# Kernel optimization log

Measured on AMD Instinct MI355X. Metric: run time of the kernel, lower is better.

Reference implementation:

```python
import jax, jax.numpy as jnp
import numpy as np

B, NQ, S, D = 8, 1024, 2048, 512

def setup_inputs() -> dict:
    key = jax.random.key(0)
    k1, k2, k3, k4 = jax.random.split(key, 4)
    queries = jax.random.normal(k1, (B, NQ, D), dtype=jnp.float32)
    keys = jax.random.normal(k2, (B, S, D), dtype=jnp.float32)
    values = jax.random.normal(k3, (B, S, D), dtype=jnp.float32)
    mask = jax.random.randint(k4, (B, NQ, S), 0, 2, dtype=jnp.int32)
    return {"queries": queries, "keys": keys, "values": values, "mask": mask}

def reference(queries, keys, values, mask):
    # scores: dot-product attention scores (b, nq, s)
    scores = jnp.einsum('bqd,bsd->bqs', queries, keys)
    attention_dist = jax.nn.softmax(scores, axis=2)
    # mask then renormalize over seq axis
    attention_dist = attention_dist * mask.astype(attention_dist.dtype)
    attention_dist = attention_dist / attention_dist.sum(axis=2, keepdims=True)
    # weighted sum of values: equivalent to (dist.unsqueeze(3) * values.unsqueeze(1)).sum(2)
    final_vector = jnp.einsum('bqs,bsd->bqd', attention_dist, values)
    return final_vector
```

## Files before the change

### kernel.cpp

```cpp
#include <hip/hip_runtime.h>


#define Bz 8
#define NQz 1024
#define Sz 2048
#define Dz 512
#define QTT 128
#define TS 32
#define KP 520
#define PP 40

typedef _Float16 f16x8 __attribute__((ext_vector_type(8)));
typedef float f32x4 __attribute__((ext_vector_type(4)));
typedef unsigned short ushort_t;

#define AS1(p) ((const __attribute__((address_space(1))) unsigned int*)(p))
#define AS3(p) ((__attribute__((address_space(3))) unsigned int*)(p))
#define DRAIN_ALL() __builtin_amdgcn_s_waitcnt(0)

__device__ __forceinline__ ushort_t f2h(float x) {
  _Float16 h = (_Float16)x;
  return __builtin_bit_cast(ushort_t, h);
}
__device__ __forceinline__ float h2f(ushort_t u) {
  return (float)__builtin_bit_cast(_Float16, u);
}

__global__ __launch_bounds__(256)
void prep(const float* __restrict__ K, const float* __restrict__ V,
          const int* __restrict__ Mi, ushort_t* __restrict__ Kf,
          ushort_t* __restrict__ Vt, unsigned* __restrict__ Mp) {
  __shared__ ushort_t sT[64][41];
  const int t = threadIdx.x;
  int bx = blockIdx.x;
  if (bx < 8192) {
    size_t e = ((size_t)bx * 256 + t) * 4;
    float4 v = *(const float4*)(K + e);
    uint2 w;
    w.x = (unsigned)f2h(v.x) | ((unsigned)f2h(v.y) << 16);
    w.y = (unsigned)f2h(v.z) | ((unsigned)f2h(v.w) << 16);
    *(uint2*)(Kf + e) = w;
    return;
  }
  bx -= 8192;
  if (bx < 4096) {
    const int b = bx >> 9;
    const int rest = bx & 511;
    const int st = rest >> 4;
    const int dt = rest & 15;
    const int s0 = st * 64, d0 = dt * 32;
    const float* Vb = V + ((size_t)b * Sz + s0) * Dz + d0;
#pragma unroll
    for (int i = 0; i < 2; ++i) {
      int idx = t + 256 * i;
      int s = idx >> 3;
      int dc = (idx & 7) * 4;
      float4 v = *(const float4*)(Vb + (size_t)s * Dz + dc);
      uint2 w;
      w.x = (unsigned)f2h(v.x) | ((unsigned)f2h(v.y) << 16);
      w.y = (unsigned)f2h(v.z) | ((unsigned)f2h(v.w) << 16);
      *(uint2*)(&sT[s][dc]) = w;
    }
    __syncthreads();
    ushort_t* VtB = Vt + ((size_t)b * Dz + d0) * Sz + s0;
    int d = t >> 3, c = t & 7;
    uint4 u;
    ushort_t* tp = (ushort_t*)&u;
#pragma unroll
    for (int j = 0; j < 8; ++j) tp[j] = sT[c * 8 + j][d];
    *(uint4*)(VtB + (size_t)d * Sz + c * 8) = u;
    return;
  }
  bx -= 4096;
  const int lane = t & 63;
  const size_t base = (size_t)bx * 1024 + t * 4;
  const int4 mv = *(const int4*)(Mi + base);
  unsigned nib = (mv.x ? 1u : 0u) | (mv.y ? 2u : 0u) |
                 (mv.z ? 4u : 0u) | (mv.w ? 8u : 0u);
  unsigned v = nib << ((lane & 7) * 4);
  v |= __shfl_xor(v, 1);
  v |= __shfl_xor(v, 2);
  v |= __shfl_xor(v, 4);
  if ((lane & 7) == 0) Mp[bx * 32 + (t >> 3)] = v;
}

template <int SPLIT>
__global__ __launch_bounds__(512, 2)
void attn_flash(const float* __restrict__ Q, const unsigned* __restrict__ Mp,
                const ushort_t* __restrict__ Kf, const ushort_t* __restrict__ Vt,
                ushort_t* __restrict__ Opart, float* __restrict__ Mpart,
                float* __restrict__ Lpart) {
  __shared__ ushort_t sK[2][TS][KP];
  __shared__ ushort_t sV[2][Dz][TS];
  __shared__ ushort_t sP[8][16][PP];

  const int tid  = threadIdx.x;
  const int wave = tid >> 6;
  const int lane = tid & 63;
  const int l16  = lane & 15;
  const int quad = lane >> 4;

  const int bxr = blockIdx.x;
  const int b   = bxr & 7;
  const int rest = bxr >> 3;
  const int qt  = rest / SPLIT;
  const int sh  = rest % SPLIT;
  const int q0  = qt * QTT;
  const int SLEN = Sz / SPLIT;
  const int NTt  = SLEN / TS;
  const int sbeg = sh * SLEN;
  const int qw   = q0 + wave * 16;

  const float*    Qb  = Q  + ((size_t)b * NQz + qw) * Dz;
  const ushort_t* KfB = Kf + (size_t)b * Sz * Dz;
  const ushort_t* VtB = Vt + (size_t)b * Dz * Sz;
  const unsigned* MpB = Mp + ((size_t)b * NQz + qw) * (Sz / 32);

  const int vql  = (lane & 3) ^ ((lane >> 3) & 3);
  const int vcol = (quad ^ ((l16 >> 1) & 3)) * 8;

  auto issue_tile = [&](int s0n, int bsel) {
#pragma unroll
    for (int j = 0; j < 4; ++j) {
      int row = wave * 4 + j;
      const ushort_t* gp = KfB + (size_t)(s0n + row) * Dz + lane * 8;
      __builtin_amdgcn_global_load_lds(AS1(gp), AS3(&sK[bsel][row][0]), 16, 0, 0);
    }
#pragma unroll
    for (int j = 0; j < 4; ++j) {
      int dbase = wave * 64 + j * 16;
      int d = dbase + (lane >> 2);
      const ushort_t* gp = VtB + (size_t)d * Sz + s0n + vql * 8;
      __builtin_amdgcn_global_load_lds(AS1(gp), AS3(&sV[bsel][dbase][0]), 16, 0, 0);
    }
  };
  auto load_mask = [&](int s0n) -> unsigned {
    return MpB[(size_t)l16 * (Sz / 32) + (s0n >> 5)];
  };

  issue_tile(sbeg, 0);
  unsigned msk_cur = load_mask(sbeg);

  f16x8 qa[16];
  {
    const float* qrow = Qb + (size_t)l16 * Dz;
#pragma unroll
    for (int kk = 0; kk < 16; ++kk) {
      const float4 a = *(const float4*)(qrow + kk * 32 + quad * 8);
      const float4 c = *(const float4*)(qrow + kk * 32 + quad * 8 + 4);
      f16x8 h;
      h[0] = (_Float16)a.x; h[1] = (_Float16)a.y;
      h[2] = (_Float16)a.z; h[3] = (_Float16)a.w;
      h[4] = (_Float16)c.x; h[5] = (_Float16)c.y;
      h[6] = (_Float16)c.z; h[7] = (_Float16)c.w;
      qa[kk] = h;
    }
  }
  if (NTt > 1) issue_tile(sbeg + TS, 1);
  DRAIN_ALL();
  __syncthreads();

  float m_ln = -1e30f, l_ln = 0.0f;
  f32x4 oacc[32];
#pragma unroll
  for (int nt = 0; nt < 32; ++nt) oacc[nt] = (f32x4){0.f, 0.f, 0.f, 0.f};

  const ushort_t* vbase0 = &sV[0][0][0] + (size_t)l16 * TS + vcol;
  const ushort_t* vbase1 = &sV[1][0][0] + (size_t)l16 * TS + vcol;

  for (int i = 0; i < NTt; ++i) {
    const int buf = i & 1;
    if (i) {
      DRAIN_ALL();
      __syncthreads();
      if (i + 1 < NTt) issue_tile(sbeg + (i + 1) * TS, buf ^ 1);
    }
    unsigned msk_nxt = (i + 1 < NTt) ? load_mask(sbeg + (i + 1) * TS) : 0u;

    f32x4 a00 = (f32x4){0.f,0.f,0.f,0.f}, a01 = (f32x4){0.f,0.f,0.f,0.f};
    f32x4 a10 = (f32x4){0.f,0.f,0.f,0.f}, a11 = (f32x4){0.f,0.f,0.f,0.f};
    {
      const ushort_t* kh0 = &sK[buf][l16][quad * 8];
      const ushort_t* kh1 = &sK[buf][16 + l16][quad * 8];
#pragma unroll
      for (int kk = 0; kk < 16; kk += 2) {
        f16x8 k00 = *(const f16x8*)(kh0 + kk * 32);
        f16x8 k10 = *(const f16x8*)(kh1 + kk * 32);
        f16x8 k01 = *(const f16x8*)(kh0 + kk * 32 + 32);
        f16x8 k11 = *(const f16x8*)(kh1 + kk * 32 + 32);
        a00 = __builtin_amdgcn_mfma_f32_16x16x32_f16(k00, qa[kk], a00, 0, 0, 0);
        a10 = __builtin_amdgcn_mfma_f32_16x16x32_f16(k10, qa[kk], a10, 0, 0, 0);
        a01 = __builtin_amdgcn_mfma_f32_16x16x32_f16(k01, qa[kk+1], a01, 0, 0, 0);
        a11 = __builtin_amdgcn_mfma_f32_16x16x32_f16(k11, qa[kk+1], a11, 0, 0, 0);
      }
    }
    f32x4 s0v, s1v;
#pragma unroll
    for (int r = 0; r < 4; ++r) { s0v[r] = a00[r] + a01[r]; s1v[r] = a10[r] + a11[r]; }

    const unsigned mb = msk_cur;
    float se0[4], se1[4];
#pragma unroll
    for (int r = 0; r < 4; ++r) {
      se0[r] = ((mb >> (quad * 4 + r)) & 1u)      ? s0v[r] : -1e30f;
      se1[r] = ((mb >> (16 + quad * 4 + r)) & 1u) ? s1v[r] : -1e30f;
    }
    float rmax = fmaxf(fmaxf(fmaxf(se0[0], se0[1]), fmaxf(se0[2], se0[3])),
                       fmaxf(fmaxf(se1[0], se1[1]), fmaxf(se1[2], se1[3])));
    rmax = fmaxf(rmax, __shfl_xor(rmax, 16));
    rmax = fmaxf(rmax, __shfl_xor(rmax, 32));

    ushort_t pb0[4], pb1[4];
    float rsum = 0.f;
#pragma unroll
    for (int r = 0; r < 4; ++r) {
      float p0 = ((mb >> (quad * 4 + r)) & 1u)      ? __expf(se0[r] - rmax) : 0.f;
      float p1 = ((mb >> (16 + quad * 4 + r)) & 1u) ? __expf(se1[r] - rmax) : 0.f;
      pb0[r] = f2h(p0); pb1[r] = f2h(p1);
      rsum += h2f(pb0[r]) + h2f(pb1[r]);
    }
    {
      uint2 w0, w1;
      w0.x = (unsigned)pb0[0] | ((unsigned)pb0[1] << 16);
      w0.y = (unsigned)pb0[2] | ((unsigned)pb0[3] << 16);
      w1.x = (unsigned)pb1[0] | ((unsigned)pb1[1] << 16);
      w1.y = (unsigned)pb1[2] | ((unsigned)pb1[3] << 16);
      *(uint2*)(&sP[wave][l16][quad * 4]) = w0;
      *(uint2*)(&sP[wave][l16][16 + quad * 4]) = w1;
    }
    rsum += __shfl_xor(rsum, 16);
    rsum += __shfl_xor(rsum, 32);

    float m_new = fmaxf(m_ln, rmax);
    float scl   = __expf(rmax - m_new);
    float al_ln = __expf(m_ln - m_new);
    bool  grw   = m_new > m_ln;
    l_ln = al_ln * l_ln + scl * rsum;
    m_ln = m_new;

    f16x8 praw = *(const f16x8*)(&sP[wave][l16][quad * 8]);
    f16x8 pa;
    {
      _Float16 sh16 = (_Float16)scl;
#pragma unroll
      for (int j = 0; j < 8; ++j) pa[j] = praw[j] * sh16;
    }

    if (__any((int)grw)) {
      float al[4];
#pragma unroll
      for (int r = 0; r < 4; ++r) al[r] = __shfl(al_ln, quad * 4 + r);
#pragma unroll
      for (int nt = 0; nt < 32; ++nt)
#pragma unroll
        for (int r = 0; r < 4; ++r) oacc[nt][r] *= al[r];
    }

    const ushort_t* vb_ = buf ? vbase1 : vbase0;
#pragma unroll
    for (int nt = 0; nt < 32; ++nt) {
      f16x8 vb = *(const f16x8*)(vb_ + nt * 512);
      oacc[nt] = __builtin_amdgcn_mfma_f32_16x16x32_f16(pa, vb, oacc[nt], 0, 0, 0);
    }

    msk_cur = msk_nxt;
  }

  const size_t rbase = (size_t)(b * SPLIT + sh) * NQz + q0 + wave * 16;
#pragma unroll
  for (int nt = 0; nt < 32; ++nt) {
#pragma unroll
    for (int r = 0; r < 4; ++r) {
      Opart[(rbase + quad * 4 + r) * Dz + nt * 16 + l16] = f2h(oacc[nt][r]);
    }
  }
  if (quad == 0) {
    Mpart[rbase + l16] = m_ln;
    Lpart[rbase + l16] = l_ln;
  }
}

template <int SPLIT>
__global__ __launch_bounds__(256)
void combine(const ushort_t* __restrict__ Opart, const float* __restrict__ Mpart,
             const float* __restrict__ Lpart, float* __restrict__ Out) {
  int gid = blockIdx.x * 256 + threadIdx.x;
  int row = gid >> 7;
  int b   = row >> 10;
  int q   = row & 1023;
  int c   = (gid & 127) * 4;
  float mv[SPLIT], lv[SPLIT];
  float m = -1e30f;
#pragma unroll
  for (int p = 0; p < SPLIT; ++p) {
    size_t ip = (size_t)(b * SPLIT + p) * NQz + q;
    mv[p] = Mpart[ip];
    lv[p] = Lpart[ip];
    m = fmaxf(m, mv[p]);
  }
  float w[SPLIT], denom = 0.f;
#pragma unroll
  for (int p = 0; p < SPLIT; ++p) {
    w[p] = __expf(mv[p] - m);
    denom += w[p] * lv[p];
  }
  float inv = 1.0f / denom;
  float4 o = {0.f, 0.f, 0.f, 0.f};
#pragma unroll
  for (int p = 0; p < SPLIT; ++p) {
    size_t ip = (size_t)(b * SPLIT + p) * NQz + q;
    const ushort_t* op = Opart + ip * Dz + c;
    uint2 raw = *(const uint2*)op;
    o.x += w[p] * h2f((ushort_t)(raw.x & 0xffff));
    o.y += w[p] * h2f((ushort_t)(raw.x >> 16));
    o.z += w[p] * h2f((ushort_t)(raw.y & 0xffff));
    o.w += w[p] * h2f((ushort_t)(raw.y >> 16));
  }
  o.x *= inv; o.y *= inv; o.z *= inv; o.w *= inv;
  *(float4*)(Out + ((size_t)b * NQz + q) * Dz + c) = o;
}

extern "C" void kernel_launch(void* const* d_in, const int* in_sizes, int n_in,
                              void* d_out, int out_size, void* d_ws, size_t ws_size,
                              hipStream_t stream) {
  const float* Q = (const float*)d_in[0];
  const float* K = (const float*)d_in[1];
  const float* V = (const float*)d_in[2];
  const int*   M = (const int*)d_in[3];
  float* O = (float*)d_out;

  const size_t NKV   = (size_t)Bz * Sz * Dz;
  const size_t maskW = (size_t)Bz * NQz * (Sz / 32);

  ushort_t* Kf = (ushort_t*)d_ws;
  ushort_t* Vt = Kf + NKV;
  unsigned* Mp = (unsigned*)(Vt + NKV);
  ushort_t* Opart = (ushort_t*)(Mp + maskW);

  auto need_bytes = [&](int S) -> size_t {
    return NKV * 2 * 2 + maskW * 4
         + (size_t)Bz * S * NQz * Dz * 2
         + (size_t)Bz * S * NQz * 4 * 2;
  };

  prep<<<dim3(28672), dim3(256), 0, stream>>>(K, V, M, Kf, Vt, Mp);

  if (ws_size >= need_bytes(4)) {
    constexpr int S = 4;
    float* Mpart = (float*)(Opart + (size_t)Bz * S * NQz * Dz);
    float* Lpart = Mpart + (size_t)Bz * S * NQz;
    attn_flash<S><<<dim3(8 * (NQz / QTT) * S), dim3(512), 0, stream>>>(
        Q, Mp, Kf, Vt, Opart, Mpart, Lpart);
    combine<S><<<dim3(4096), dim3(256), 0, stream>>>(Opart, Mpart, Lpart, O);
  } else {
    constexpr int S = 2;
    float* Mpart = (float*)(Opart + (size_t)Bz * S * NQz * Dz);
    float* Lpart = Mpart + (size_t)Bz * S * NQz;
    attn_flash<S><<<dim3(8 * (NQz / QTT) * S), dim3(512), 0, stream>>>(
        Q, Mp, Kf, Vt, Opart, Mpart, Lpart);
    combine<S><<<dim3(4096), dim3(256), 0, stream>>>(Opart, Mpart, Lpart, O);
  }
}
```

Before: 246.7 us.

## Shrink flash tiles to 16 keys, keep P in registers with 16x16x16 MFMA

Halves the query tile (4 waves of 16 rows) and the key tile (16 keys), so the PV product can take P directly from the QK accumulator layout via the 16x16x16 f16 MFMA. This removes the per-wave shared-memory round trip for P. The mask word is now loaded every other tile, softmax scaling uses the running max directly, and MFMA sections are wrapped in s_setprio. The trade-off is smaller tiles: twice as many barrier iterations, and K/V tiles are reused by fewer query rows per block, which raises LDS and global traffic per FLOP. The smaller MFMA shape also does less work per instruction.

```diff
diff --git a/kernel.cpp b/kernel.cpp
--- a/kernel.cpp
+++ b/kernel.cpp
@@ -5,12 +5,12 @@
 #define NQz 1024
 #define Sz 2048
 #define Dz 512
-#define QTT 128
-#define TS 32
+#define QTT 64
+#define TS 16
 #define KP 520
-#define PP 40
 
 typedef _Float16 f16x8 __attribute__((ext_vector_type(8)));
+typedef _Float16 f16x4 __attribute__((ext_vector_type(4)));
 typedef float f32x4 __attribute__((ext_vector_type(4)));
 typedef unsigned short ushort_t;
 
@@ -85,14 +85,13 @@
 }
 
 template <int SPLIT>
-__global__ __launch_bounds__(512, 2)
+__global__ __launch_bounds__(256, 2)
 void attn_flash(const float* __restrict__ Q, const unsigned* __restrict__ Mp,
                 const ushort_t* __restrict__ Kf, const ushort_t* __restrict__ Vt,
                 ushort_t* __restrict__ Opart, float* __restrict__ Mpart,
                 float* __restrict__ Lpart) {
   __shared__ ushort_t sK[2][TS][KP];
   __shared__ ushort_t sV[2][Dz][TS];
-  __shared__ ushort_t sP[8][16][PP];
 
   const int tid  = threadIdx.x;
   const int wave = tid >> 6;
@@ -116,9 +115,6 @@
   const ushort_t* VtB = Vt + (size_t)b * Dz * Sz;
   const unsigned* MpB = Mp + ((size_t)b * NQz + qw) * (Sz / 32);
 
-  const int vql  = (lane & 3) ^ ((lane >> 3) & 3);
-  const int vcol = (quad ^ ((l16 >> 1) & 3)) * 8;
-
   auto issue_tile = [&](int s0n, int bsel) {
 #pragma unroll
     for (int j = 0; j < 4; ++j) {
@@ -128,18 +124,15 @@
     }
 #pragma unroll
     for (int j = 0; j < 4; ++j) {
-      int dbase = wave * 64 + j * 16;
-      int d = dbase + (lane >> 2);
-      const ushort_t* gp = VtB + (size_t)d * Sz + s0n + vql * 8;
+      int dbase = wave * 128 + j * 32;
+      int d = dbase + (lane >> 1);
+      const ushort_t* gp = VtB + (size_t)d * Sz + s0n + (lane & 1) * 8;
       __builtin_amdgcn_global_load_lds(AS1(gp), AS3(&sV[bsel][dbase][0]), 16, 0, 0);
     }
   };
-  auto load_mask = [&](int s0n) -> unsigned {
-    return MpB[(size_t)l16 * (Sz / 32) + (s0n >> 5)];
-  };
 
   issue_tile(sbeg, 0);
-  unsigned msk_cur = load_mask(sbeg);
+  unsigned msk_word = MpB[(size_t)l16 * (Sz / 32) + (sbeg >> 5)];
 
   f16x8 qa[16];
   {
@@ -165,9 +158,7 @@
 #pragma unroll
   for (int nt = 0; nt < 32; ++nt) oacc[nt] = (f32x4){0.f, 0.f, 0.f, 0.f};
 
-  const ushort_t* vbase0 = &sV[0][0][0] + (size_t)l16 * TS + vcol;
-  const ushort_t* vbase1 = &sV[1][0][0] + (size_t)l16 * TS + vcol;
-
+  unsigned msk_nxt = 0;
   for (int i = 0; i < NTt; ++i) {
     const int buf = i & 1;
     if (i) {
@@ -175,97 +166,77 @@
       __syncthreads();
       if (i + 1 < NTt) issue_tile(sbeg + (i + 1) * TS, buf ^ 1);
     }
-    unsigned msk_nxt = (i + 1 < NTt) ? load_mask(sbeg + (i + 1) * TS) : 0u;
-
-    f32x4 a00 = (f32x4){0.f,0.f,0.f,0.f}, a01 = (f32x4){0.f,0.f,0.f,0.f};
-    f32x4 a10 = (f32x4){0.f,0.f,0.f,0.f}, a11 = (f32x4){0.f,0.f,0.f,0.f};
+    if ((i & 1) && (i + 1 < NTt))
+      msk_nxt = MpB[(size_t)l16 * (Sz / 32) + ((sbeg + (i + 1) * TS) >> 5)];
+
+    f32x4 a0 = (f32x4){0.f, 0.f, 0.f, 0.f};
+    f32x4 a1 = (f32x4){0.f, 0.f, 0.f, 0.f};
     {
-      const ushort_t* kh0 = &sK[buf][l16][quad * 8];
-      const ushort_t* kh1 = &sK[buf][16 + l16][quad * 8];
+      const ushort_t* kh = &sK[buf][l16][quad * 8];
+      __builtin_amdgcn_s_setprio(1);
 #pragma unroll
       for (int kk = 0; kk < 16; kk += 2) {
-        f16x8 k00 = *(const f16x8*)(kh0 + kk * 32);
-        f16x8 k10 = *(const f16x8*)(kh1 + kk * 32);
-        f16x8 k01 = *(const f16x8*)(kh0 + kk * 32 + 32);
-        f16x8 k11 = *(const f16x8*)(kh1 + kk * 32 + 32);
-        a00 = __builtin_amdgcn_mfma_f32_16x16x32_f16(k00, qa[kk], a00, 0, 0, 0);
-        a10 = __builtin_amdgcn_mfma_f32_16x16x32_f16(k10, qa[kk], a10, 0, 0, 0);
-        a01 = __builtin_amdgcn_mfma_f32_16x16x32_f16(k01, qa[kk+1], a01, 0, 0, 0);
-        a11 = __builtin_amdgcn_mfma_f32_16x16x32_f16(k11, qa[kk+1], a11, 0, 0, 0);
+        f16x8 k0 = *(const f16x8*)(kh + kk * 32);
+        f16x8 k1 = *(const f16x8*)(kh + kk * 32 + 32);
+        a0 = __builtin_amdgcn_mfma_f32_16x16x32_f16(k0, qa[kk], a0, 0, 0, 0);
+        a1 = __builtin_amdgcn_mfma_f32_16x16x32_f16(k1, qa[kk + 1], a1, 0, 0, 0);
       }
-    }
-    f32x4 s0v, s1v;
-#pragma unroll
-    for (int r = 0; r < 4; ++r) { s0v[r] = a00[r] + a01[r]; s1v[r] = a10[r] + a11[r]; }
-
-    const unsigned mb = msk_cur;
-    float se0[4], se1[4];
-#pragma unroll
-    for (int r = 0; r < 4; ++r) {
-      se0[r] = ((mb >> (quad * 4 + r)) & 1u)      ? s0v[r] : -1e30f;
-      se1[r] = ((mb >> (16 + quad * 4 + r)) & 1u) ? s1v[r] : -1e30f;
-    }
-    float rmax = fmaxf(fmaxf(fmaxf(se0[0], se0[1]), fmaxf(se0[2], se0[3])),
-                       fmaxf(fmaxf(se1[0], se1[1]), fmaxf(se1[2], se1[3])));
+      __builtin_amdgcn_s_setprio(0);
+    }
+    f32x4 sc;
+#pragma unroll
+    for (int r = 0; r < 4; ++r) sc[r] = a0[r] + a1[r];
+
+    const unsigned mbits = msk_word >> (((i & 1) << 4) + quad * 4);
+    float se[4];
+#pragma unroll
+    for (int r = 0; r < 4; ++r) se[r] = ((mbits >> r) & 1u) ? sc[r] : -1e30f;
+    float rmax = fmaxf(fmaxf(se[0], se[1]), fmaxf(se[2], se[3]));
     rmax = fmaxf(rmax, __shfl_xor(rmax, 16));
     rmax = fmaxf(rmax, __shfl_xor(rmax, 32));
-
-    ushort_t pb0[4], pb1[4];
+    float m_new = fmaxf(m_ln, rmax);
+    float al    = __expf(m_ln - m_new);
+    bool  grw   = m_new > m_ln;
+
+    f16x4 pa;
     float rsum = 0.f;
 #pragma unroll
     for (int r = 0; r < 4; ++r) {
-      float p0 = ((mb >> (quad * 4 + r)) & 1u)      ? __expf(se0[r] - rmax) : 0.f;
-      float p1 = ((mb >> (16 + quad * 4 + r)) & 1u) ? __expf(se1[r] - rmax) : 0.f;
-      pb0[r] = f2h(p0); pb1[r] = f2h(p1);
-      rsum += h2f(pb0[r]) + h2f(pb1[r]);
-    }
-    {
-      uint2 w0, w1;
-      w0.x = (unsigned)pb0[0] | ((unsigned)pb0[1] << 16);
-      w0.y = (unsigned)pb0[2] | ((unsigned)pb0[3] << 16);
-      w1.x = (unsigned)pb1[0] | ((unsigned)pb1[1] << 16);
-      w1.y = (unsigned)pb1[2] | ((unsigned)pb1[3] << 16);
-      *(uint2*)(&sP[wave][l16][quad * 4]) = w0;
-      *(uint2*)(&sP[wave][l16][16 + quad * 4]) = w1;
+      float p = ((mbits >> r) & 1u) ? __expf(se[r] - m_new) : 0.f;
+      ushort_t ph = f2h(p);
+      pa[r] = __builtin_bit_cast(_Float16, ph);
+      rsum += h2f(ph);
     }
     rsum += __shfl_xor(rsum, 16);
     rsum += __shfl_xor(rsum, 32);
-
-    float m_new = fmaxf(m_ln, rmax);
-    float scl   = __expf(rmax - m_new);
-    float al_ln = __expf(m_ln - m_new);
-    bool  grw   = m_new > m_ln;
-    l_ln = al_ln * l_ln + scl * rsum;
+    l_ln = al * l_ln + rsum;
     m_ln = m_new;
 
-    f16x8 praw = *(const f16x8*)(&sP[wave][l16][quad * 8]);
-    f16x8 pa;
+    if (__any((int)grw)) {
+      float alr[4];
+#pragma unroll
+      for (int r = 0; r < 4; ++r) alr[r] = __shfl(al, quad * 4 + r);
+#pragma unroll
+      for (int nt = 0; nt < 32; ++nt)
+#pragma unroll
+        for (int r = 0; r < 4; ++r) oacc[nt][r] *= alr[r];
+    }
+
     {
-      _Float16 sh16 = (_Float16)scl;
-#pragma unroll
-      for (int j = 0; j < 8; ++j) pa[j] = praw[j] * sh16;
-    }
-
-    if (__any((int)grw)) {
-      float al[4];
-#pragma unroll
-      for (int r = 0; r < 4; ++r) al[r] = __shfl(al_ln, quad * 4 + r);
-#pragma unroll
-      for (int nt = 0; nt < 32; ++nt)
-#pragma unroll
-        for (int r = 0; r < 4; ++r) oacc[nt][r] *= al[r];
-    }
-
-    const ushort_t* vb_ = buf ? vbase1 : vbase0;
-#pragma unroll
-    for (int nt = 0; nt < 32; ++nt) {
-      f16x8 vb = *(const f16x8*)(vb_ + nt * 512);
-      oacc[nt] = __builtin_amdgcn_mfma_f32_16x16x32_f16(pa, vb, oacc[nt], 0, 0, 0);
-    }
-
-    msk_cur = msk_nxt;
-  }
-
+      const ushort_t* vb_ = &sV[buf][0][0] + l16 * 16 + quad * 4;
+      __builtin_amdgcn_s_setprio(1);
+#pragma unroll
+      for (int nt = 0; nt < 32; ++nt) {
+        f16x4 vb = *(const f16x4*)(vb_ + nt * 256);
+        oacc[nt] = __builtin_amdgcn_mfma_f32_16x16x16f16(pa, vb, oacc[nt], 0, 0, 0);
+      }
+      __builtin_amdgcn_s_setprio(0);
+    }
+
+    if (i & 1) msk_word = msk_nxt;
+  }
+
+  DRAIN_ALL();
   const size_t rbase = (size_t)(b * SPLIT + sh) * NQz + q0 + wave * 16;
 #pragma unroll
   for (int nt = 0; nt < 32; ++nt) {
@@ -349,14 +320,14 @@
     constexpr int S = 4;
     float* Mpart = (float*)(Opart + (size_t)Bz * S * NQz * Dz);
     float* Lpart = Mpart + (size_t)Bz * S * NQz;
-    attn_flash<S><<<dim3(8 * (NQz / QTT) * S), dim3(512), 0, stream>>>(
+    attn_flash<S><<<dim3(8 * (NQz / QTT) * S), dim3(256), 0, stream>>>(
         Q, Mp, Kf, Vt, Opart, Mpart, Lpart);
     combine<S><<<dim3(4096), dim3(256), 0, stream>>>(Opart, Mpart, Lpart, O);
   } else {
     constexpr int S = 2;
     float* Mpart = (float*)(Opart + (size_t)Bz * S * NQz * Dz);
     float* Lpart = Mpart + (size_t)Bz * S * NQz;
-    attn_flash<S><<<dim3(8 * (NQz / QTT) * S), dim3(512), 0, stream>>>(
+    attn_flash<S><<<dim3(8 * (NQz / QTT) * S), dim3(256), 0, stream>>>(
         Q, Mp, Kf, Vt, Opart, Mpart, Lpart);
     combine<S><<<dim3(4096), dim3(256), 0, stream>>>(Opart, Mpart, Lpart, O);
   }
```

After: 277.4 us. +12.4%, slower.

## Shrink query tile to 64 rows and replace double buffering with split K/V prefetch

Applied to the files above, without the earlier changes.

Halves the query tile per block (4 waves, 256 threads) and drops the double-buffered K/V shared-memory tiles in favour of a single buffer. The next K tile is loaded while the PV product runs, and the next V tile is loaded after it, each guarded by a vmcnt wait plus barrier. MFMA loops are wrapped in s_setprio to favour math waves. Less LDS per block should allow more resident blocks, but each block reloads K/V for fewer queries and takes two barriers per tile.

```diff
diff --git a/kernel.cpp b/kernel.cpp
--- a/kernel.cpp
+++ b/kernel.cpp
@@ -5,7 +5,7 @@
 #define NQz 1024
 #define Sz 2048
 #define Dz 512
-#define QTT 128
+#define QTT 64
 #define TS 32
 #define KP 520
 #define PP 40
@@ -17,6 +17,12 @@
 #define AS1(p) ((const __attribute__((address_space(1))) unsigned int*)(p))
 #define AS3(p) ((__attribute__((address_space(3))) unsigned int*)(p))
 #define DRAIN_ALL() __builtin_amdgcn_s_waitcnt(0)
+#define DRAIN_BAR()                                         \
+  do {                                                      \
+    asm volatile("s_waitcnt vmcnt(0)" ::: "memory");        \
+    __builtin_amdgcn_s_barrier();                           \
+    asm volatile("" ::: "memory");                          \
+  } while (0)
 
 __device__ __forceinline__ ushort_t f2h(float x) {
   _Float16 h = (_Float16)x;
@@ -85,14 +91,14 @@
 }
 
 template <int SPLIT>
-__global__ __launch_bounds__(512, 2)
+__global__ __launch_bounds__(256, 2)
 void attn_flash(const float* __restrict__ Q, const unsigned* __restrict__ Mp,
                 const ushort_t* __restrict__ Kf, const ushort_t* __restrict__ Vt,
                 ushort_t* __restrict__ Opart, float* __restrict__ Mpart,
                 float* __restrict__ Lpart) {
-  __shared__ ushort_t sK[2][TS][KP];
-  __shared__ ushort_t sV[2][Dz][TS];
-  __shared__ ushort_t sP[8][16][PP];
+  __shared__ ushort_t sK[TS][KP];
+  __shared__ ushort_t sV[Dz][TS];
+  __shared__ ushort_t sP[4][16][PP];
 
   const int tid  = threadIdx.x;
   const int wave = tid >> 6;
@@ -119,27 +125,27 @@
   const int vql  = (lane & 3) ^ ((lane >> 3) & 3);
   const int vcol = (quad ^ ((l16 >> 1) & 3)) * 8;
 
-  auto issue_tile = [&](int s0n, int bsel) {
-#pragma unroll
-    for (int j = 0; j < 4; ++j) {
-      int row = wave * 4 + j;
+  auto issue_k = [&](int s0n) {
+#pragma unroll
+    for (int j = 0; j < 8; ++j) {
+      int row = wave * 8 + j;
       const ushort_t* gp = KfB + (size_t)(s0n + row) * Dz + lane * 8;
-      __builtin_amdgcn_global_load_lds(AS1(gp), AS3(&sK[bsel][row][0]), 16, 0, 0);
-    }
-#pragma unroll
-    for (int j = 0; j < 4; ++j) {
-      int dbase = wave * 64 + j * 16;
+      __builtin_amdgcn_global_load_lds(AS1(gp), AS3(&sK[row][0]), 16, 0, 0);
+    }
+  };
+  auto issue_v = [&](int s0n) {
+#pragma unroll
+    for (int j = 0; j < 8; ++j) {
+      int dbase = wave * 128 + j * 16;
       int d = dbase + (lane >> 2);
       const ushort_t* gp = VtB + (size_t)d * Sz + s0n + vql * 8;
-      __builtin_amdgcn_global_load_lds(AS1(gp), AS3(&sV[bsel][dbase][0]), 16, 0, 0);
+      __builtin_amdgcn_global_load_lds(AS1(gp), AS3(&sV[dbase][0]), 16, 0, 0);
     }
   };
-  auto load_mask = [&](int s0n) -> unsigned {
-    return MpB[(size_t)l16 * (Sz / 32) + (s0n >> 5)];
-  };
-
-  issue_tile(sbeg, 0);
-  unsigned msk_cur = load_mask(sbeg);
+
+  issue_k(sbeg);
+  issue_v(sbeg);
+  unsigned msk_cur = MpB[(size_t)l16 * (Sz / 32) + (sbeg >> 5)];
 
   f16x8 qa[16];
   {
@@ -156,7 +162,6 @@
       qa[kk] = h;
     }
   }
-  if (NTt > 1) issue_tile(sbeg + TS, 1);
   DRAIN_ALL();
   __syncthreads();
 
@@ -165,23 +170,13 @@
 #pragma unroll
   for (int nt = 0; nt < 32; ++nt) oacc[nt] = (f32x4){0.f, 0.f, 0.f, 0.f};
 
-  const ushort_t* vbase0 = &sV[0][0][0] + (size_t)l16 * TS + vcol;
-  const ushort_t* vbase1 = &sV[1][0][0] + (size_t)l16 * TS + vcol;
-
   for (int i = 0; i < NTt; ++i) {
-    const int buf = i & 1;
-    if (i) {
-      DRAIN_ALL();
-      __syncthreads();
-      if (i + 1 < NTt) issue_tile(sbeg + (i + 1) * TS, buf ^ 1);
-    }
-    unsigned msk_nxt = (i + 1 < NTt) ? load_mask(sbeg + (i + 1) * TS) : 0u;
-
     f32x4 a00 = (f32x4){0.f,0.f,0.f,0.f}, a01 = (f32x4){0.f,0.f,0.f,0.f};
     f32x4 a10 = (f32x4){0.f,0.f,0.f,0.f}, a11 = (f32x4){0.f,0.f,0.f,0.f};
     {
-      const ushort_t* kh0 = &sK[buf][l16][quad * 8];
-      const ushort_t* kh1 = &sK[buf][16 + l16][quad * 8];
+      const ushort_t* kh0 = &sK[l16][quad * 8];
+      const ushort_t* kh1 = &sK[16 + l16][quad * 8];
+      __builtin_amdgcn_s_setprio(1);
 #pragma unroll
       for (int kk = 0; kk < 16; kk += 2) {
         f16x8 k00 = *(const f16x8*)(kh0 + kk * 32);
@@ -193,6 +188,7 @@
         a01 = __builtin_amdgcn_mfma_f32_16x16x32_f16(k01, qa[kk+1], a01, 0, 0, 0);
         a11 = __builtin_amdgcn_mfma_f32_16x16x32_f16(k11, qa[kk+1], a11, 0, 0, 0);
       }
+      __builtin_amdgcn_s_setprio(0);
     }
     f32x4 s0v, s1v;
 #pragma unroll
@@ -238,6 +234,13 @@
     l_ln = al_ln * l_ln + scl * rsum;
     m_ln = m_new;
 
+    DRAIN_BAR();
+    unsigned msk_nxt = 0;
+    if (i + 1 < NTt) {
+      msk_nxt = MpB[(size_t)l16 * (Sz / 32) + ((sbeg + (i + 1) * TS) >> 5)];
+      issue_k(sbeg + (i + 1) * TS);
+    }
+
     f16x8 praw = *(const f16x8*)(&sP[wave][l16][quad * 8]);
     f16x8 pa;
     {
@@ -247,21 +250,28 @@
     }
 
     if (__any((int)grw)) {
-      float al[4];
-#pragma unroll
-      for (int r = 0; r < 4; ++r) al[r] = __shfl(al_ln, quad * 4 + r);
+      float alr[4];
+#pragma unroll
+      for (int r = 0; r < 4; ++r) alr[r] = __shfl(al_ln, quad * 4 + r);
 #pragma unroll
       for (int nt = 0; nt < 32; ++nt)
 #pragma unroll
-        for (int r = 0; r < 4; ++r) oacc[nt][r] *= al[r];
-    }
-
-    const ushort_t* vb_ = buf ? vbase1 : vbase0;
-#pragma unroll
-    for (int nt = 0; nt < 32; ++nt) {
-      f16x8 vb = *(const f16x8*)(vb_ + nt * 512);
-      oacc[nt] = __builtin_amdgcn_mfma_f32_16x16x32_f16(pa, vb, oacc[nt], 0, 0, 0);
-    }
+        for (int r = 0; r < 4; ++r) oacc[nt][r] *= alr[r];
+    }
+
+    {
+      const ushort_t* vb_ = &sV[0][0] + (size_t)l16 * TS + vcol;
+      __builtin_amdgcn_s_setprio(1);
+#pragma unroll
+      for (int nt = 0; nt < 32; ++nt) {
+        f16x8 vb = *(const f16x8*)(vb_ + nt * 512);
+        oacc[nt] = __builtin_amdgcn_mfma_f32_16x16x32_f16(pa, vb, oacc[nt], 0, 0, 0);
+      }
+      __builtin_amdgcn_s_setprio(0);
+    }
+
+    DRAIN_BAR();
+    if (i + 1 < NTt) issue_v(sbeg + (i + 1) * TS);
 
     msk_cur = msk_nxt;
   }
@@ -349,14 +359,14 @@
     constexpr int S = 4;
     float* Mpart = (float*)(Opart + (size_t)Bz * S * NQz * Dz);
     float* Lpart = Mpart + (size_t)Bz * S * NQz;
-    attn_flash<S><<<dim3(8 * (NQz / QTT) * S), dim3(512), 0, stream>>>(
+    attn_flash<S><<<dim3(8 * (NQz / QTT) * S), dim3(256), 0, stream>>>(
         Q, Mp, Kf, Vt, Opart, Mpart, Lpart);
     combine<S><<<dim3(4096), dim3(256), 0, stream>>>(Opart, Mpart, Lpart, O);
   } else {
     constexpr int S = 2;
     float* Mpart = (float*)(Opart + (size_t)Bz * S * NQz * Dz);
     float* Lpart = Mpart + (size_t)Bz * S * NQz;
-    attn_flash<S><<<dim3(8 * (NQz / QTT) * S), dim3(512), 0, stream>>>(
+    attn_flash<S><<<dim3(8 * (NQz / QTT) * S), dim3(256), 0, stream>>>(
         Q, Mp, Kf, Vt, Opart, Mpart, Lpart);
     combine<S><<<dim3(4096), dim3(256), 0, stream>>>(Opart, Mpart, Lpart, O);
   }
```

New measurement: 248.6 us. No clear change (+0.8%).
